# Kernel optimization log

Hardware: AMD Instinct MI355X
Metric: run time of the kernel (lower is better)

Reference implementation:

```python
import jax, jax.numpy as jnp
import numpy as np

B, S, D, H, DFF = 2, 2048, 1024, 16, 4096
DK = D // H
EPS = float(np.finfo(np.float32).eps)  # torch RMSNorm default eps = finfo eps


def rmsnorm(x, g):
    var = jnp.mean(x * x, axis=-1, keepdims=True)
    return x * jax.lax.rsqrt(var + EPS) * g


def rope_cos_sin(seq_len, dim, base=10000.0):
    inv_freq = 1.0 / (base ** (jnp.arange(0, dim, 2, dtype=jnp.float32) / dim))
    t = jnp.arange(seq_len, dtype=jnp.float32)
    freqs = jnp.outer(t, inv_freq)            # [S, dim/2]
    emb = jnp.concatenate([freqs, freqs], -1)  # [S, dim]
    return jnp.cos(emb), jnp.sin(emb)


def rotate_half(x):
    x1, x2 = x[..., : x.shape[-1] // 2], x[..., x.shape[-1] // 2:]
    return jnp.concatenate([-x2, x1], axis=-1)


def setup_inputs() -> dict:
    key = jax.random.key(0)
    ks = jax.random.split(key, 16)
    sc = 0.02
    return {
        "x": jax.random.normal(ks[0], (B, S, D), jnp.float32),
        "wq": jax.random.normal(ks[1], (D, D), jnp.float32) * sc,
        "bq": jnp.zeros((D,), jnp.float32),
        "wk": jax.random.normal(ks[2], (D, D), jnp.float32) * sc,
        "bk": jnp.zeros((D,), jnp.float32),
        "wv": jax.random.normal(ks[3], (D, D), jnp.float32) * sc,
        "bv": jnp.zeros((D,), jnp.float32),
        "wo": jax.random.normal(ks[4], (D, D), jnp.float32) * sc,
        "bo": jnp.zeros((D,), jnp.float32),
        "w1": jax.random.normal(ks[5], (D, DFF), jnp.float32) * sc,
        "b1": jnp.zeros((DFF,), jnp.float32),
        "w2": jax.random.normal(ks[6], (DFF, D), jnp.float32) * sc,
        "b2": jnp.zeros((D,), jnp.float32),
        "g1": jnp.ones((D,), jnp.float32),
        "g2": jnp.ones((D,), jnp.float32),
    }


def reference(x, wq, bq, wk, bk, wv, bv, wo, bo, w1, b1, w2, b2, g1, g2):
    b, s, d = x.shape
    # --- self-attention sublayer (pre-RMSNorm residual) ---
    h = rmsnorm(x, g1)
    q = (h @ wq + bq).reshape(b, s, H, DK).transpose(0, 2, 1, 3)  # [B,H,S,dk]
    k = (h @ wk + bk).reshape(b, s, H, DK).transpose(0, 2, 1, 3)
    v = (h @ wv + bv).reshape(b, s, H, DK).transpose(0, 2, 1, 3)
    cos, sin = rope_cos_sin(s, DK)
    cos = cos[None, None]  # [1,1,S,dk]
    sin = sin[None, None]
    q = q * cos + rotate_half(q) * sin
    k = k * cos + rotate_half(k) * sin
    scores = jnp.einsum("bhqd,bhkd->bhqk", q, k) / jnp.sqrt(jnp.float32(DK))
    p = jax.nn.softmax(scores, axis=-1)
    o = jnp.einsum("bhqk,bhkd->bhqd", p, v)
    o = o.transpose(0, 2, 1, 3).reshape(b, s, d)
    attn_out = o @ wo + bo
    x = x + attn_out
    # --- feed-forward sublayer ---
    h2 = rmsnorm(x, g2)
    ff = jax.nn.relu(h2 @ w1 + b1) @ w2 + b2
    return x + ff
```

## Files before the change

kernel.cpp:

```cpp
#include <hip/hip_runtime.h>
#include <math.h>

typedef unsigned short u16;
typedef __attribute__((ext_vector_type(8))) short bf16x8;
typedef __attribute__((ext_vector_type(4))) float f32x4;
typedef __attribute__((ext_vector_type(4))) unsigned int u32x4;

#define B_ 2
#define S_ 2048
#define D_ 1024
#define H_ 16
#define DK_ 64
#define DFF_ 4096
#define EPS_ 1.1920928955078125e-07f
#define EXP2SC 0.18033688011112042f

__device__ __forceinline__ float bf2f(u16 u) {
  unsigned int v = ((unsigned int)u) << 16;
  return __builtin_bit_cast(float, v);
}
__device__ __forceinline__ u16 f2bf(float f) {
  unsigned int x = __builtin_bit_cast(unsigned int, f);
  x += 0x7fffu + ((x >> 16) & 1u);
  return (u16)(x >> 16);
}

typedef __attribute__((address_space(3))) unsigned int lds_uint;
typedef const __attribute__((address_space(1))) unsigned int glb_uint;
__device__ __forceinline__ void gload16(const void* g, void* l) {
  __builtin_amdgcn_global_load_lds((glb_uint*)g, (lds_uint*)l, 16, 0, 0);
}

template <int N>
__device__ __forceinline__ void waitcnt_vm() {
  if constexpr (N == 8) asm volatile("s_waitcnt vmcnt(8)" ::: "memory");
  else if constexpr (N == 6) asm volatile("s_waitcnt vmcnt(6)" ::: "memory");
  else asm volatile("s_waitcnt vmcnt(0)" ::: "memory");
}

__device__ __forceinline__ unsigned int cvtpk(float lo, float hi) {
  unsigned int d;
  asm("v_cvt_pk_bf16_f32 %0, %1, %2" : "=v"(d) : "v"(lo), "v"(hi));
  return d;
}
__device__ __forceinline__ void plswap32(unsigned int& a, unsigned int& b) {
  asm("v_permlane32_swap_b32 %0, %1" : "+v"(a), "+v"(b));
}
__device__ __forceinline__ void plswap16(unsigned int& a, unsigned int& b) {
  asm("v_permlane16_swap_b32 %0, %1" : "+v"(a), "+v"(b));
}

__device__ __forceinline__ void xcd_swizzle(int& bx, int& by) {
  const int nx = gridDim.x;
  const int nwg = nx * gridDim.y;
  const int lin = blockIdx.y * nx + blockIdx.x;
  const int swz = (lin & 7) * (nwg >> 3) + (lin >> 3);
  bx = swz % nx;
  by = swz / nx;
}

__global__ __launch_bounds__(256) void prep_qkvo(
    const float* __restrict__ wq, const float* __restrict__ wk,
    const float* __restrict__ wv, const float* __restrict__ wo,
    u16* __restrict__ qkvT, u16* __restrict__ woT,
    float* __restrict__ cosT, float* __restrict__ sinT) {
  __shared__ float t[32][33];
  const int bid = blockIdx.x;
  const int tid = threadIdx.x;
  if (bid < 4096) {
    const int m = bid >> 10;
    const int tb = bid & 1023;
    const float* src = (m == 0) ? wq : (m == 1) ? wk : (m == 2) ? wv : wo;
    u16* dst = (m == 3) ? woT : qkvT + (size_t)m * D_ * D_;
    const int c0 = (tb & 31) * 32, r0 = (tb >> 5) * 32;
    const int tx = tid & 31, ty = tid >> 5;
#pragma unroll
    for (int i = 0; i < 32; i += 8)
      t[ty + i][tx] = src[(size_t)(r0 + ty + i) * D_ + (c0 + tx)];
    __syncthreads();
#pragma unroll
    for (int i = 0; i < 32; i += 8)
      dst[(size_t)(c0 + ty + i) * D_ + (r0 + tx)] = f2bf(t[tx][ty + i]);
  } else {
    const int idx = (bid - 4096) * 256 + tid;
    const int s = idx >> 5, i = idx & 31;
    double inv = exp(((double)(-2 * i) / (double)DK_) * log(10000.0));
    double ang = (double)s * inv;
    cosT[idx] = (float)cos(ang);
    sinT[idx] = (float)sin(ang);
  }
}

__global__ __launch_bounds__(256) void prep_w12(
    const float* __restrict__ w1, const float* __restrict__ w2,
    u16* __restrict__ w1T, u16* __restrict__ w2T) {
  __shared__ float t[32][33];
  const int bid = blockIdx.x;
  const int tid = threadIdx.x;
  const int tx = tid & 31, ty = tid >> 5;
  if (bid < 4096) {
    const int c0 = (bid & 127) * 32, r0 = (bid >> 7) * 32;
#pragma unroll
    for (int i = 0; i < 32; i += 8)
      t[ty + i][tx] = w1[(size_t)(r0 + ty + i) * DFF_ + (c0 + tx)];
    __syncthreads();
#pragma unroll
    for (int i = 0; i < 32; i += 8)
      w1T[(size_t)(c0 + ty + i) * D_ + (r0 + tx)] = f2bf(t[tx][ty + i]);
  } else {
    const int b2 = bid - 4096;
    const int c0 = (b2 & 31) * 32, r0 = (b2 >> 5) * 32;
#pragma unroll
    for (int i = 0; i < 32; i += 8)
      t[ty + i][tx] = w2[(size_t)(r0 + ty + i) * D_ + (c0 + tx)];
    __syncthreads();
#pragma unroll
    for (int i = 0; i < 32; i += 8)
      w2T[(size_t)(c0 + ty + i) * DFF_ + (r0 + tx)] = f2bf(t[tx][ty + i]);
  }
}

__global__ __launch_bounds__(256) void rmsnorm_k(const float* __restrict__ X,
                                                 const float* __restrict__ g,
                                                 u16* __restrict__ out) {
  const int row = blockIdx.x;
  const float* xr = X + (size_t)row * D_;
  u16* orow = out + (size_t)row * D_;
  const int tid = threadIdx.x;
  float vals[4];
  float s = 0.f;
#pragma unroll
  for (int j = 0; j < 4; j++) {
    float v = xr[tid + j * 256];
    vals[j] = v;
    s += v * v;
  }
#pragma unroll
  for (int off = 32; off > 0; off >>= 1) s += __shfl_down(s, off, 64);
  __shared__ float red[4];
  __shared__ float ssc;
  int lane = tid & 63, wave = tid >> 6;
  if (lane == 0) red[wave] = s;
  __syncthreads();
  if (tid == 0) ssc = 1.0f / sqrtf((red[0] + red[1] + red[2] + red[3]) * (1.0f / D_) + EPS_);
  __syncthreads();
  float sc = ssc;
#pragma unroll
  for (int j = 0; j < 4; j++) {
    int i = tid + j * 256;
    orow[i] = f2bf(vals[j] * sc * g[i]);
  }
}

#define GK_STAGE(BU, K0)                                                               \
  _Pragma("unroll")                                                                    \
  for (int p = 0; p < 2; p++) {                                                        \
    _Pragma("unroll")                                                                  \
    for (int c = wave; c < BM / 16; c += 4) {                                          \
      const u16* gp = gkA + (size_t)(m0 + c * 16 + lrow) * gkLD + (K0) + p * 32 + lcol; \
      gload16(gp, (char*)As + __builtin_amdgcn_readfirstlane((BU) * (BM * 128) + p * (BM * 64) + c * 1024)); \
    }                                                                                  \
    _Pragma("unroll")                                                                  \
    for (int c = wave; c < BN / 16; c += 4) {                                          \
      const u16* gp = gkB + (size_t)(n0 + c * 16 + lrow) * gkLD + (K0) + p * 32 + lcol; \
      gload16(gp, (char*)Bs + __builtin_amdgcn_readfirstlane((BU) * (BN * 128) + p * (BN * 64) + c * 1024)); \
    }                                                                                  \
  }

#define GK_COMPUTE(BU)                                                                 \
  _Pragma("unroll")                                                                    \
  for (int p = 0; p < 2; p++) {                                                        \
    bf16x8 af[WR], bfv[WC];                                                            \
    _Pragma("unroll")                                                                  \
    for (int i = 0; i < WR; i++)                                                       \
      af[i] = *(const bf16x8*)&As[(BU) * (BM * 64) + p * (BM * 32) + (wm + i * 16 + l16) * 32 + quad * 8]; \
    _Pragma("unroll")                                                                  \
    for (int j = 0; j < WC; j++)                                                       \
      bfv[j] = *(const bf16x8*)&Bs[(BU) * (BN * 64) + p * (BN * 32) + (wn + j * 16 + l16) * 32 + quad * 8]; \
    _Pragma("unroll")                                                                  \
    for (int i = 0; i < WR; i++)                                                       \
      _Pragma("unroll")                                                                \
      for (int j = 0; j < WC; j++)                                                     \
        acc[i][j] = __builtin_amdgcn_mfma_f32_16x16x32_bf16(af[i], bfv[j], acc[i][j], 0, 0, 0); \
  }

#define GEMM_KLOOP(APTR, BPTR, KLEN, KLD)                                              \
  {                                                                                    \
    const u16* gkA = (APTR);                                                           \
    const u16* gkB = (BPTR);                                                           \
    const int gkLD = (KLD);                                                            \
    GK_STAGE(0, 0)                                                                     \
    GK_STAGE(1, 64)                                                                    \
    int gkcur = 0;                                                                     \
    for (int k0 = 0; k0 < (KLEN); k0 += 64) {                                          \
      if (k0 + 64 < (KLEN)) waitcnt_vm<WR + WC>();   \
      else waitcnt_vm<0>();                                      \
      __builtin_amdgcn_s_barrier();                                                    \
      GK_COMPUTE(gkcur)                                                                \
      __builtin_amdgcn_s_barrier();                         \
      if (k0 + 128 < (KLEN)) { GK_STAGE(gkcur, k0 + 128) }                             \
      gkcur ^= 1;                                                                      \
    }                                                                                  \
  }

template <int MODE, int WR, int WC>
__global__ __launch_bounds__(256) void gemm_bt(
    const u16* __restrict__ A, const u16* __restrict__ Bt, const float* __restrict__ bias,
    u16* __restrict__ outB, float* __restrict__ outF, const float* __restrict__ resF,
    int M, int N, int K) {
  constexpr int BM = 2 * WR * 16;
  constexpr int BN = 2 * WC * 16;
  __shared__ u16 As[2 * BM * 64];
  __shared__ u16 Bs[2 * BN * 64];
  const int tid = threadIdx.x;
  const int wave = tid >> 6, lane = tid & 63, quad = lane >> 4, l16 = lane & 15;
  const int wm = (wave >> 1) * (WR * 16), wn = (wave & 1) * (WC * 16);
  int bx, by;
  xcd_swizzle(bx, by);
  const int m0 = by * BM, n0 = bx * BN;
  const int lrow = lane >> 2, lcol = (lane & 3) * 8;
  f32x4 acc[WR][WC] = {};
  GEMM_KLOOP(A, Bt, K, K)
#pragma unroll
  for (int i = 0; i < WR; i++)
#pragma unroll
    for (int j = 0; j < WC; j++) {
      int col = n0 + wn + j * 16 + l16;
      float bv = bias[col];
#pragma unroll
      for (int r = 0; r < 4; r++) {
        int row = m0 + wm + i * 16 + quad * 4 + r;
        size_t off = (size_t)row * N + col;
        float v = acc[i][j][r] + bv;
        if constexpr (MODE == 1) v = fmaxf(v, 0.f);
        if constexpr (MODE == 2) outF[off] = v + resF[off];
        else outB[off] = f2bf(v);
      }
    }
}

__global__ __launch_bounds__(256) void gemm_qkv(
    const u16* __restrict__ A, const u16* __restrict__ Bt,
    const float* __restrict__ bq, const float* __restrict__ bk, const float* __restrict__ bv,
    const float* __restrict__ cosT, const float* __restrict__ sinT,
    u16* __restrict__ Qb, u16* __restrict__ Kb, u16* __restrict__ VT, int M, int K) {
  constexpr int WR = 4, WC = 4;
  constexpr int BM = 128, BN = 128;
  __shared__ u16 As[2 * BM * 64];
  __shared__ u16 Bs[2 * BN * 64];
  const int tid = threadIdx.x;
  const int wave = tid >> 6, lane = tid & 63, quad = lane >> 4, l16 = lane & 15;
  const int wm = (wave >> 1) * 64, wn = (wave & 1) * 64;
  int bx, by;
  xcd_swizzle(bx, by);
  const int m0 = by * BM, n0 = bx * BN;
  const int lrow = lane >> 2, lcol = (lane & 3) * 8;
  f32x4 acc[WR][WC] = {};
  GEMM_KLOOP(A, Bt, K, K)
  const int g = n0 >> 10;
  if (g < 2) {
    u16* dst = (g == 0) ? Qb : Kb;
    const float* bias = (g == 0) ? bq : bk;
    const float scq = (g == 0) ? EXP2SC : 1.0f;
#pragma unroll
    for (int i = 0; i < WR; i++)
#pragma unroll
      for (int jp = 0; jp < 2; jp++) {
        int col0 = n0 + wn + jp * 16 + l16;
        int c0 = col0 & 1023;
        float bv0 = bias[c0], bv1 = bias[c0 + 32];
        int irot = jp * 16 + l16;
        int row0 = m0 + wm + i * 16 + quad * 4;
#pragma unroll
        for (int r = 0; r < 4; r++) {
          int row = row0 + r;
          int s2 = row & 2047;
          float cs = cosT[s2 * 32 + irot];
          float sn = sinT[s2 * 32 + irot];
          float x0 = acc[i][jp][r] + bv0;
          float x1 = acc[i][jp + 2][r] + bv1;
          dst[(size_t)row * D_ + c0]      = f2bf((x0 * cs - x1 * sn) * scq);
          dst[(size_t)row * D_ + c0 + 32] = f2bf((x1 * cs + x0 * sn) * scq);
        }
      }
  } else {
#pragma unroll
    for (int i = 0; i < WR; i++)
#pragma unroll
      for (int j = 0; j < WC; j++) {
        int col = n0 + wn + j * 16 + l16;
        int c = col & 1023;
        float bvv = bv[c];
        int row0 = m0 + wm + i * 16 + quad * 4;
        int hh = c >> 6, dk = c & 63;
        int b = row0 >> 11, s2 = row0 & 2047;
        ushort4 pv;
        pv.x = f2bf(acc[i][j][0] + bvv);
        pv.y = f2bf(acc[i][j][1] + bvv);
        pv.z = f2bf(acc[i][j][2] + bvv);
        pv.w = f2bf(acc[i][j][3] + bvv);
        *(ushort4*)&VT[(((size_t)(b * H_ + hh)) * DK_ + dk) * S_ + s2] = pv;
      }
  }
}

template <int WR, int WC>
__global__ __launch_bounds__(256) void gemm_splitk(
    const u16* __restrict__ A, const u16* __restrict__ Bt, const float* __restrict__ bias,
    float* outF, int M, int N, int Kslice, int Kld) {
  constexpr int BM = 2 * WR * 16;
  constexpr int BN = 2 * WC * 16;
  __shared__ u16 As[2 * BM * 64];
  __shared__ u16 Bs[2 * BN * 64];
  const int tid = threadIdx.x;
  const int wave = tid >> 6, lane = tid & 63, quad = lane >> 4, l16 = lane & 15;
  const int wm = (wave >> 1) * (WR * 16), wn = (wave & 1) * (WC * 16);
  int bx, by;
  xcd_swizzle(bx, by);
  const int m0 = by * BM, n0 = bx * BN;
  const int lrow = lane >> 2, lcol = (lane & 3) * 8;
  const u16* Ao = A + (size_t)blockIdx.z * Kslice;
  const u16* Bo = Bt + (size_t)blockIdx.z * Kslice;
  f32x4 acc[WR][WC] = {};
  GEMM_KLOOP(Ao, Bo, Kslice, Kld)
  const bool addb = (blockIdx.z == 0);
#pragma unroll
  for (int i = 0; i < WR; i++)
#pragma unroll
    for (int j = 0; j < WC; j++) {
      int col = n0 + wn + j * 16 + l16;
      float bv = addb ? bias[col] : 0.f;
#pragma unroll
      for (int r = 0; r < 4; r++) {
        int row = m0 + wm + i * 16 + quad * 4 + r;
        unsafeAtomicAdd(&outF[(size_t)row * N + col], acc[i][j][r] + bv);
      }
    }
}

__device__ __forceinline__ void softmax_pack(f32x4 s0, f32x4 s1, f32x4 s2, f32x4 s3,
                                             bf16x8& pf0, bf16x8& pf1) {
  f32x4 p0, p1, p2, p3;
#pragma unroll
  for (int r = 0; r < 4; r++) {
    p0[r] = exp2f(s0[r]);
    p1[r] = exp2f(s1[r]);
    p2[r] = exp2f(s2[r]);
    p3[r] = exp2f(s3[r]);
  }
  unsigned int X0 = cvtpk(p0[0], p0[1]), X1 = cvtpk(p0[2], p0[3]);
  unsigned int Y0 = cvtpk(p1[0], p1[1]), Y1 = cvtpk(p1[2], p1[3]);
  unsigned int Z0 = cvtpk(p2[0], p2[1]), Z1 = cvtpk(p2[2], p2[3]);
  unsigned int W0 = cvtpk(p3[0], p3[1]), W1 = cvtpk(p3[2], p3[3]);
  plswap32(X0, Y0); plswap16(X0, Y0);
  plswap32(X1, Y1); plswap16(X1, Y1);
  plswap32(Z0, W0); plswap16(Z0, W0);
  plswap32(Z1, W1); plswap16(Z1, W1);
  u32x4 lo = {X0, X1, Y0, Y1};
  u32x4 hi = {Z0, Z1, W0, W1};
  pf0 = __builtin_bit_cast(bf16x8, lo);
  pf1 = __builtin_bit_cast(bf16x8, hi);
}

__global__ __launch_bounds__(256, 2) void flash_attn(u16* __restrict__ Q,
                                                     const u16* __restrict__ Kg,
                                                     const u16* __restrict__ VT) {
  const int bh = blockIdx.y;
  const int b = bh >> 4, h = bh & 15;
  const int q0 = blockIdx.x * 128;
  const int tid = threadIdx.x;
  const int wave = tid >> 6, lane = tid & 63, quad = lane >> 4, l16 = lane & 15;
  const size_t base = (size_t)b * S_ * D_ + h * DK_;
  const size_t vbase = (size_t)bh * DK_ * S_;

  __shared__ u16 Ks[2][8192];
  __shared__ u16 Vts[2][8192];

  const int kkey = wave * 32 + (lane >> 3);
  const int kcol = ((lane & 7) ^ (lane >> 3)) * 8;
  const u16* kp0 = Kg + base + (size_t)kkey * D_ + kcol;
  const int vdk0 = wave * 16 + (lane >> 4);
  const int vsel = lane & 15;
  const u16* vp0 = VT + vbase + (size_t)vdk0 * S_;

#define STAGE(BU, KT)                                                                  \
  _Pragma("unroll")                                                                    \
  for (int c = 0; c < 4; c++) {                                                        \
    gload16(kp0 + (size_t)((KT) + c * 8) * D_,                                         \
            (char*)Ks + __builtin_amdgcn_readfirstlane((BU) * 16384 + wave * 4096 + c * 1024)); \
    int vdk = vdk0 + c * 4;                                                            \
    gload16(vp0 + (size_t)(c * 4) * S_ + (KT) + ((vsel ^ (vdk & 7)) * 8),              \
            (char*)Vts + __builtin_amdgcn_readfirstlane((BU) * 16384 + wave * 4096 + c * 1024)); \
  }

  STAGE(0, 0)

  const size_t qoffA = base + (size_t)(q0 + wave * 32 + l16) * D_ + quad * 8;
  const size_t qoffB = qoffA + (size_t)16 * D_;
  bf16x8 qa0 = *(const bf16x8*)(Q + qoffA);
  bf16x8 qa1 = *(const bf16x8*)(Q + qoffA + 32);
  bf16x8 qb0 = *(const bf16x8*)(Q + qoffB);
  bf16x8 qb1 = *(const bf16x8*)(Q + qoffB + 32);

  f32x4 oa[4] = {}, ob[4] = {};
  f32x4 lsa_acc = {}, lsb_acc = {};
  const u32x4 onesu = {0x3F803F80u, 0x3F803F80u, 0x3F803F80u, 0x3F803F80u};
  const bf16x8 ones = __builtin_bit_cast(bf16x8, onesu);
  const int sw = (l16 & 7) << 4;

#define TILE(BU)                                                                       \
  {                                                                                    \
    const char* KsB = (const char*)Ks + (BU) * 16384;                                  \
    const char* VtsB = (const char*)Vts + (BU) * 16384;                                \
    f32x4 sa[2][4] = {}, sb[2][4] = {};                                                \
    __builtin_amdgcn_s_setprio(1);                                                     \
    _Pragma("unroll")                                                                  \
    for (int half = 0; half < 2; half++) {                                             \
      _Pragma("unroll")                                                                \
      for (int nt = 0; nt < 4; nt++) {                                                 \
        const int kr = half * 64 + nt * 16 + l16;                                      \
        const char* krow = KsB + kr * 128;                                             \
        bf16x8 k0 = *(const bf16x8*)(krow + ((quad * 16) ^ sw));                       \
        bf16x8 k1 = *(const bf16x8*)(krow + ((64 + quad * 16) ^ sw));                  \
        sa[half][nt] = __builtin_amdgcn_mfma_f32_16x16x32_bf16(k0, qa0, sa[half][nt], 0, 0, 0); \
        sa[half][nt] = __builtin_amdgcn_mfma_f32_16x16x32_bf16(k1, qa1, sa[half][nt], 0, 0, 0); \
        sb[half][nt] = __builtin_amdgcn_mfma_f32_16x16x32_bf16(k0, qb0, sb[half][nt], 0, 0, 0); \
        sb[half][nt] = __builtin_amdgcn_mfma_f32_16x16x32_bf16(k1, qb1, sb[half][nt], 0, 0, 0); \
      }                                                                                \
    }                                                                                  \
    __builtin_amdgcn_s_setprio(0);                                                     \
    bf16x8 pa[2][2], pb[2][2];                                                         \
    _Pragma("unroll")                                                                  \
    for (int half = 0; half < 2; half++) {                                             \
      softmax_pack(sa[half][0], sa[half][1], sa[half][2], sa[half][3], pa[half][0], pa[half][1]); \
      softmax_pack(sb[half][0], sb[half][1], sb[half][2], sb[half][3], pb[half][0], pb[half][1]); \
    }                                                                                  \
    __builtin_amdgcn_s_setprio(1);                                                     \
    _Pragma("unroll")                                                                  \
    for (int half = 0; half < 2; half++) {                                             \
      lsa_acc = __builtin_amdgcn_mfma_f32_16x16x32_bf16(pa[half][0], ones, lsa_acc, 0, 0, 0); \
      lsa_acc = __builtin_amdgcn_mfma_f32_16x16x32_bf16(pa[half][1], ones, lsa_acc, 0, 0, 0); \
      lsb_acc = __builtin_amdgcn_mfma_f32_16x16x32_bf16(pb[half][0], ones, lsb_acc, 0, 0, 0); \
      lsb_acc = __builtin_amdgcn_mfma_f32_16x16x32_bf16(pb[half][1], ones, lsb_acc, 0, 0, 0); \
      _Pragma("unroll")                                                                \
      for (int nt = 0; nt < 4; nt++) {                                                 \
        const int vr = nt * 16 + l16;                                                  \
        const char* vrow = VtsB + vr * 256;                                            \
        bf16x8 v0 = *(const bf16x8*)(vrow + ((half * 128 + quad * 16) ^ sw));          \
        bf16x8 v1 = *(const bf16x8*)(vrow + ((half * 128 + 64 + quad * 16) ^ sw));     \
        oa[nt] = __builtin_amdgcn_mfma_f32_16x16x32_bf16(pa[half][0], v0, oa[nt], 0, 0, 0); \
        oa[nt] = __builtin_amdgcn_mfma_f32_16x16x32_bf16(pa[half][1], v1, oa[nt], 0, 0, 0); \
        ob[nt] = __builtin_amdgcn_mfma_f32_16x16x32_bf16(pb[half][0], v0, ob[nt], 0, 0, 0); \
        ob[nt] = __builtin_amdgcn_mfma_f32_16x16x32_bf16(pb[half][1], v1, ob[nt], 0, 0, 0); \
      }                                                                                \
    }                                                                                  \
    __builtin_amdgcn_s_setprio(0);                                                     \
  }

  for (int kt = 0; kt < S_; kt += 256) {
    __syncthreads();
    STAGE(1, kt + 128)
    TILE(0)
    __syncthreads();
    if (kt + 256 < S_) { STAGE(0, kt + 256) }
    TILE(1)
  }
#undef STAGE
#undef TILE

#pragma unroll
  for (int r = 0; r < 4; r++) {
    float inva = 1.0f / lsa_acc[r];
    float invb = 1.0f / lsb_acc[r];
    const size_t aoff = base + (size_t)(q0 + wave * 32 + quad * 4 + r) * D_;
    const size_t boff = aoff + (size_t)16 * D_;
#pragma unroll
    for (int nt = 0; nt < 4; nt++) {
      Q[aoff + nt * 16 + l16] = f2bf(oa[nt][r] * inva);
      Q[boff + nt * 16 + l16] = f2bf(ob[nt][r] * invb);
    }
  }
}

extern "C" void kernel_launch(void* const* d_in, const int* in_sizes, int n_in,
                              void* d_out, int out_size, void* d_ws, size_t ws_size,
                              hipStream_t stream) {
  const float* x  = (const float*)d_in[0];
  const float* wq = (const float*)d_in[1];
  const float* bq = (const float*)d_in[2];
  const float* wk = (const float*)d_in[3];
  const float* bk = (const float*)d_in[4];
  const float* wv = (const float*)d_in[5];
  const float* bv = (const float*)d_in[6];
  const float* wo = (const float*)d_in[7];
  const float* bo = (const float*)d_in[8];
  const float* w1 = (const float*)d_in[9];
  const float* b1 = (const float*)d_in[10];
  const float* w2 = (const float*)d_in[11];
  const float* b2 = (const float*)d_in[12];
  const float* g1 = (const float*)d_in[13];
  const float* g2 = (const float*)d_in[14];

  char* ws = (char*)d_ws;
  const size_t MB = 1024 * 1024;
  u16* qkvT = (u16*)(ws + 0 * MB);
  u16* woT  = (u16*)(ws + 6 * MB);
  u16* h    = (u16*)(ws + 8 * MB);
  u16* Qb   = (u16*)(ws + 16 * MB);
  u16* Kb   = (u16*)(ws + 24 * MB);
  float* cosT = (float*)(ws + 32 * MB);
  float* sinT = (float*)(ws + 32 * MB + 256 * 1024);
  u16* w2T  = (u16*)(ws + 0 * MB);
  u16* w1T  = (u16*)(ws + 16 * MB);
  u16* f1   = (u16*)(ws + 24 * MB);
  u16* h2   = h;
  u16* Ob   = Qb;
  u16* VT   = (u16*)d_out;
  float* x2 = (float*)d_out;
  const bool bigffn = (ws_size >= 57 * MB);

  const int MS = B_ * S_;
  prep_qkvo<<<4096 + S_ * 32 / 256, 256, 0, stream>>>(wq, wk, wv, wo, qkvT, woT, cosT, sinT);
  rmsnorm_k<<<MS, 256, 0, stream>>>(x, g1, h);
  gemm_qkv<<<dim3(3 * D_ / 128, MS / 128), 256, 0, stream>>>(h, qkvT, bq, bk, bv, cosT, sinT, Qb, Kb, VT, MS, D_);
  flash_attn<<<dim3(S_ / 128, B_ * H_), 256, 0, stream>>>(Qb, Kb, VT);
  gemm_bt<2, 4, 2><<<dim3(D_ / 64, MS / 128), 256, 0, stream>>>(Ob, woT, bo, nullptr, x2, x, MS, D_, D_);

  prep_w12<<<8192, 256, 0, stream>>>(w1, w2, w1T, w2T);
  rmsnorm_k<<<MS, 256, 0, stream>>>(x2, g2, h2);
  if (bigffn) {
    gemm_bt<1, 4, 4><<<dim3(DFF_ / 128, MS / 128), 256, 0, stream>>>(h2, w1T, b1, f1, nullptr, nullptr, MS, DFF_, D_);
    gemm_splitk<4, 4><<<dim3(D_ / 128, MS / 128, 2), 256, 0, stream>>>(f1, w2T, b2, x2, MS, D_, 2048, DFF_);
  } else {
    for (int i = 0; i < 2; i++) {
      const u16* h2h = h2 + (size_t)i * 2048 * D_;
      float* x2h = x2 + (size_t)i * 2048 * D_;
      gemm_bt<1, 4, 4><<<dim3(DFF_ / 128, 2048 / 128), 256, 0, stream>>>(h2h, w1T, b1, f1, nullptr, nullptr, 2048, DFF_, D_);
      gemm_splitk<4, 4><<<dim3(D_ / 128, 2048 / 128, 4), 256, 0, stream>>>(f1, w2T, b2, x2h, 2048, D_, 1024, DFF_);
    }
  }
  (void)in_sizes; (void)n_in; (void)out_size;
}
```

Before: 363.3 us.

## Shrink flash-attention key tiles to 64 with deeper prefetch and higher occupancy

The flash attention kernel now processes 64-key tiles instead of 128-key ones. LDS buffers are halved and launch bounds go from 2 to 4 blocks per CU, aiming to hide latency through occupancy. Synchronisation changes from __syncthreads to explicit vmcnt waits plus s_barrier, which keeps one stage of prefetch in flight, and exp2f is swapped for the raw hardware exp2 builtin. The costs are more barriers per key, tighter register limits that may cause spills, and reduced exp2 accuracy.

```diff
diff --git a/kernel.cpp b/kernel.cpp
--- a/kernel.cpp
+++ b/kernel.cpp
@@ -25,6 +25,12 @@
   return (u16)(x >> 16);
 }
 
+#if __has_builtin(__builtin_amdgcn_exp2f)
+__device__ __forceinline__ float exp2r(float x) { return __builtin_amdgcn_exp2f(x); }
+#else
+__device__ __forceinline__ float exp2r(float x) { return exp2f(x); }
+#endif
+
 typedef __attribute__((address_space(3))) unsigned int lds_uint;
 typedef const __attribute__((address_space(1))) unsigned int glb_uint;
 __device__ __forceinline__ void gload16(const void* g, void* l) {
@@ -35,6 +41,7 @@
 __device__ __forceinline__ void waitcnt_vm() {
   if constexpr (N == 8) asm volatile("s_waitcnt vmcnt(8)" ::: "memory");
   else if constexpr (N == 6) asm volatile("s_waitcnt vmcnt(6)" ::: "memory");
+  else if constexpr (N == 4) asm volatile("s_waitcnt vmcnt(4)" ::: "memory");
   else asm volatile("s_waitcnt vmcnt(0)" ::: "memory");
 }
 
@@ -343,10 +350,10 @@
   f32x4 p0, p1, p2, p3;
 #pragma unroll
   for (int r = 0; r < 4; r++) {
-    p0[r] = exp2f(s0[r]);
-    p1[r] = exp2f(s1[r]);
-    p2[r] = exp2f(s2[r]);
-    p3[r] = exp2f(s3[r]);
+    p0[r] = exp2r(s0[r]);
+    p1[r] = exp2r(s1[r]);
+    p2[r] = exp2r(s2[r]);
+    p3[r] = exp2r(s3[r]);
   }
   unsigned int X0 = cvtpk(p0[0], p0[1]), X1 = cvtpk(p0[2], p0[3]);
   unsigned int Y0 = cvtpk(p1[0], p1[1]), Y1 = cvtpk(p1[2], p1[3]);
@@ -362,7 +369,7 @@
   pf1 = __builtin_bit_cast(bf16x8, hi);
 }
 
-__global__ __launch_bounds__(256, 2) void flash_attn(u16* __restrict__ Q,
+__global__ __launch_bounds__(256, 4) void flash_attn(u16* __restrict__ Q,
                                                      const u16* __restrict__ Kg,
                                                      const u16* __restrict__ VT) {
   const int bh = blockIdx.y;
@@ -373,27 +380,27 @@
   const size_t base = (size_t)b * S_ * D_ + h * DK_;
   const size_t vbase = (size_t)bh * DK_ * S_;
 
-  __shared__ u16 Ks[2][8192];
-  __shared__ u16 Vts[2][8192];
-
-  const int kkey = wave * 32 + (lane >> 3);
-  const int kcol = ((lane & 7) ^ (lane >> 3)) * 8;
-  const u16* kp0 = Kg + base + (size_t)kkey * D_ + kcol;
-  const int vdk0 = wave * 16 + (lane >> 4);
-  const int vsel = lane & 15;
-  const u16* vp0 = VT + vbase + (size_t)vdk0 * S_;
-
-#define STAGE(BU, KT)                                                                  \
+  __shared__ u16 Ks[2][4096];
+  __shared__ u16 Vts[2][4096];
+
+  const int srow8 = lane >> 3;
+  const int scol = ((lane & 7) ^ srow8) * 8;
+  const int kkey = wave * 16 + srow8;
+  const u16* kp0 = Kg + base + (size_t)kkey * D_ + scol;
+  const int vdk = wave * 16 + srow8;
+  const u16* vp0 = VT + vbase + (size_t)vdk * S_ + scol;
+
+#define FA_STAGE(BU, KT)                                                               \
   _Pragma("unroll")                                                                    \
-  for (int c = 0; c < 4; c++) {                                                        \
+  for (int c = 0; c < 2; c++) {                                                        \
     gload16(kp0 + (size_t)((KT) + c * 8) * D_,                                         \
-            (char*)Ks + __builtin_amdgcn_readfirstlane((BU) * 16384 + wave * 4096 + c * 1024)); \
-    int vdk = vdk0 + c * 4;                                                            \
-    gload16(vp0 + (size_t)(c * 4) * S_ + (KT) + ((vsel ^ (vdk & 7)) * 8),              \
-            (char*)Vts + __builtin_amdgcn_readfirstlane((BU) * 16384 + wave * 4096 + c * 1024)); \
-  }
-
-  STAGE(0, 0)
+            (char*)Ks + __builtin_amdgcn_readfirstlane((BU) * 8192 + wave * 2048 + c * 1024)); \
+    gload16(vp0 + (size_t)(c * 8) * S_ + (KT),                                         \
+            (char*)Vts + __builtin_amdgcn_readfirstlane((BU) * 8192 + wave * 2048 + c * 1024)); \
+  }
+
+  FA_STAGE(0, 0)
+  FA_STAGE(1, 64)
 
   const size_t qoffA = base + (size_t)(q0 + wave * 32 + l16) * D_ + quad * 8;
   const size_t qoffB = qoffA + (size_t)16 * D_;
@@ -408,65 +415,56 @@
   const bf16x8 ones = __builtin_bit_cast(bf16x8, onesu);
   const int sw = (l16 & 7) << 4;
 
-#define TILE(BU)                                                                       \
+#define FA_TILE(BU)                                                                    \
   {                                                                                    \
-    const char* KsB = (const char*)Ks + (BU) * 16384;                                  \
-    const char* VtsB = (const char*)Vts + (BU) * 16384;                                \
-    f32x4 sa[2][4] = {}, sb[2][4] = {};                                                \
+    const char* KsB = (const char*)Ks + (BU) * 8192;                                   \
+    const char* VtsB = (const char*)Vts + (BU) * 8192;                                 \
+    f32x4 sa[4] = {}, sb[4] = {};                                                      \
     __builtin_amdgcn_s_setprio(1);                                                     \
     _Pragma("unroll")                                                                  \
-    for (int half = 0; half < 2; half++) {                                             \
-      _Pragma("unroll")                                                                \
-      for (int nt = 0; nt < 4; nt++) {                                                 \
-        const int kr = half * 64 + nt * 16 + l16;                                      \
-        const char* krow = KsB + kr * 128;                                             \
-        bf16x8 k0 = *(const bf16x8*)(krow + ((quad * 16) ^ sw));                       \
-        bf16x8 k1 = *(const bf16x8*)(krow + ((64 + quad * 16) ^ sw));                  \
-        sa[half][nt] = __builtin_amdgcn_mfma_f32_16x16x32_bf16(k0, qa0, sa[half][nt], 0, 0, 0); \
-        sa[half][nt] = __builtin_amdgcn_mfma_f32_16x16x32_bf16(k1, qa1, sa[half][nt], 0, 0, 0); \
-        sb[half][nt] = __builtin_amdgcn_mfma_f32_16x16x32_bf16(k0, qb0, sb[half][nt], 0, 0, 0); \
-        sb[half][nt] = __builtin_amdgcn_mfma_f32_16x16x32_bf16(k1, qb1, sb[half][nt], 0, 0, 0); \
-      }                                                                                \
+    for (int nt = 0; nt < 4; nt++) {                                                   \
+      const char* krow = KsB + (nt * 16 + l16) * 128;                                  \
+      bf16x8 k0 = *(const bf16x8*)(krow + ((quad * 16) ^ sw));                         \
+      bf16x8 k1 = *(const bf16x8*)(krow + ((64 + quad * 16) ^ sw));                    \
+      sa[nt] = __builtin_amdgcn_mfma_f32_16x16x32_bf16(k0, qa0, sa[nt], 0, 0, 0);      \
+      sa[nt] = __builtin_amdgcn_mfma_f32_16x16x32_bf16(k1, qa1, sa[nt], 0, 0, 0);      \
+      sb[nt] = __builtin_amdgcn_mfma_f32_16x16x32_bf16(k0, qb0, sb[nt], 0, 0, 0);      \
+      sb[nt] = __builtin_amdgcn_mfma_f32_16x16x32_bf16(k1, qb1, sb[nt], 0, 0, 0);      \
     }                                                                                  \
     __builtin_amdgcn_s_setprio(0);                                                     \
-    bf16x8 pa[2][2], pb[2][2];                                                         \
-    _Pragma("unroll")                                                                  \
-    for (int half = 0; half < 2; half++) {                                             \
-      softmax_pack(sa[half][0], sa[half][1], sa[half][2], sa[half][3], pa[half][0], pa[half][1]); \
-      softmax_pack(sb[half][0], sb[half][1], sb[half][2], sb[half][3], pb[half][0], pb[half][1]); \
-    }                                                                                  \
+    bf16x8 pa0, pa1, pb0, pb1;                                                         \
+    softmax_pack(sa[0], sa[1], sa[2], sa[3], pa0, pa1);                                \
+    softmax_pack(sb[0], sb[1], sb[2], sb[3], pb0, pb1);                                \
     __builtin_amdgcn_s_setprio(1);                                                     \
-    _Pragma("unroll")                                                                  \
-    for (int half = 0; half < 2; half++) {                                             \
-      lsa_acc = __builtin_amdgcn_mfma_f32_16x16x32_bf16(pa[half][0], ones, lsa_acc, 0, 0, 0); \
-      lsa_acc = __builtin_amdgcn_mfma_f32_16x16x32_bf16(pa[half][1], ones, lsa_acc, 0, 0, 0); \
-      lsb_acc = __builtin_amdgcn_mfma_f32_16x16x32_bf16(pb[half][0], ones, lsb_acc, 0, 0, 0); \
-      lsb_acc = __builtin_amdgcn_mfma_f32_16x16x32_bf16(pb[half][1], ones, lsb_acc, 0, 0, 0); \
-      _Pragma("unroll")                                                                \
-      for (int nt = 0; nt < 4; nt++) {                                                 \
-        const int vr = nt * 16 + l16;                                                  \
-        const char* vrow = VtsB + vr * 256;                                            \
-        bf16x8 v0 = *(const bf16x8*)(vrow + ((half * 128 + quad * 16) ^ sw));          \
-        bf16x8 v1 = *(const bf16x8*)(vrow + ((half * 128 + 64 + quad * 16) ^ sw));     \
-        oa[nt] = __builtin_amdgcn_mfma_f32_16x16x32_bf16(pa[half][0], v0, oa[nt], 0, 0, 0); \
-        oa[nt] = __builtin_amdgcn_mfma_f32_16x16x32_bf16(pa[half][1], v1, oa[nt], 0, 0, 0); \
-        ob[nt] = __builtin_amdgcn_mfma_f32_16x16x32_bf16(pb[half][0], v0, ob[nt], 0, 0, 0); \
-        ob[nt] = __builtin_amdgcn_mfma_f32_16x16x32_bf16(pb[half][1], v1, ob[nt], 0, 0, 0); \
-      }                                                                                \
+    lsa_acc = __builtin_amdgcn_mfma_f32_16x16x32_bf16(pa0, ones, lsa_acc, 0, 0, 0);    \
+    lsa_acc = __builtin_amdgcn_mfma_f32_16x16x32_bf16(pa1, ones, lsa_acc, 0, 0, 0);    \
+    lsb_acc = __builtin_amdgcn_mfma_f32_16x16x32_bf16(pb0, ones, lsb_acc, 0, 0, 0);    \
+    lsb_acc = __builtin_amdgcn_mfma_f32_16x16x32_bf16(pb1, ones, lsb_acc, 0, 0, 0);    \
+    _Pragma("unroll")                                                                  \
+    for (int nt = 0; nt < 4; nt++) {                                                   \
+      const char* vrow = VtsB + (nt * 16 + l16) * 128;                                 \
+      bf16x8 v0 = *(const bf16x8*)(vrow + ((quad * 16) ^ sw));                         \
+      bf16x8 v1 = *(const bf16x8*)(vrow + ((64 + quad * 16) ^ sw));                    \
+      oa[nt] = __builtin_amdgcn_mfma_f32_16x16x32_bf16(pa0, v0, oa[nt], 0, 0, 0);      \
+      oa[nt] = __builtin_amdgcn_mfma_f32_16x16x32_bf16(pa1, v1, oa[nt], 0, 0, 0);      \
+      ob[nt] = __builtin_amdgcn_mfma_f32_16x16x32_bf16(pb0, v0, ob[nt], 0, 0, 0);      \
+      ob[nt] = __builtin_amdgcn_mfma_f32_16x16x32_bf16(pb1, v1, ob[nt], 0, 0, 0);      \
     }                                                                                  \
     __builtin_amdgcn_s_setprio(0);                                                     \
   }
 
-  for (int kt = 0; kt < S_; kt += 256) {
-    __syncthreads();
-    STAGE(1, kt + 128)
-    TILE(0)
-    __syncthreads();
-    if (kt + 256 < S_) { STAGE(0, kt + 256) }
-    TILE(1)
-  }
-#undef STAGE
-#undef TILE
+  int cur = 0;
+  for (int kt = 0; kt < S_; kt += 64) {
+    if (kt + 64 < S_) waitcnt_vm<4>();
+    else waitcnt_vm<0>();
+    __builtin_amdgcn_s_barrier();
+    FA_TILE(cur)
+    __builtin_amdgcn_s_barrier();
+    if (kt + 128 < S_) { FA_STAGE(cur, kt + 128) }
+    cur ^= 1;
+  }
+#undef FA_STAGE
+#undef FA_TILE
 
 #pragma unroll
   for (int r = 0; r < 4; r++) {
```

Result: faster. 348.9 us (-4.0%).
